# Kernel optimization log

Measured on AMD Instinct MI355X. Metric: run time of the kernel, lower is better.

The kernel has to match this reference:

```python
import jax, jax.numpy as jnp
import numpy as np

TEMP = 1.0  # temperature

def setup_inputs() -> dict:
    key = jax.random.key(0)
    ks = jax.random.split(key, 16)
    B, Cin, Cout, H, W, K, kk, A = 32, 64, 64, 128, 128, 4, 3, 16
    c_ = Cin + Cout
    r = lambda k, s: jax.random.normal(k, s, dtype=jnp.float32)
    return {
        'x': r(ks[0], (B, Cin, H, W)),
        'fc_w': r(ks[1], (A, Cin)) * 0.1,
        'ch_w': r(ks[2], (Cin, A)) * 0.1,
        'ch_b': jnp.zeros((Cin,), jnp.float32),
        'f_w': r(ks[3], (Cout, A)) * 0.1,
        'f_b': jnp.zeros((Cout,), jnp.float32),
        'sp_w': r(ks[4], (kk * kk, A)) * 0.1,
        'sp_b': jnp.zeros((kk * kk,), jnp.float32),
        'k_w': r(ks[5], (K, A)) * 0.1,
        'k_b': jnp.zeros((K,), jnp.float32),
        'fus_w1': r(ks[6], (c_ // 16, c_)) * 0.1,
        'fus_b1': jnp.zeros((c_ // 16,), jnp.float32),
        'fus_w2': r(ks[7], (c_, c_ // 16)) * 0.1,
        'fus_b2': jnp.zeros((c_,), jnp.float32),
        'weight': r(ks[8], (K, Cout, Cin, kk, kk)) * (1.0 / np.sqrt(Cin * kk * kk)),
    }

def reference(x, fc_w, ch_w, ch_b, f_w, f_b, sp_w, sp_b, k_w, k_b,
              fus_w1, fus_b1, fus_w2, fus_b2, weight):
    B, Cin, H, W = x.shape
    K, Cout, _, kk, _ = weight.shape
    # --- Attention branches (on globally pooled features) ---
    pooled = x.mean(axis=(2, 3))                      # (B, Cin)
    a = jax.nn.relu(pooled @ fc_w.T)                  # (B, A)
    ch_att = jax.nn.sigmoid(a @ ch_w.T + ch_b)        # (B, Cin)
    f_att = jax.nn.sigmoid(a @ f_w.T + f_b)           # (B, Cout)
    sp_att = jax.nn.sigmoid(a @ sp_w.T + sp_b).reshape(B, 1, 1, 1, kk, kk)
    k_att = jax.nn.softmax((a @ k_w.T + k_b) / TEMP, axis=1).reshape(B, K, 1, 1, 1, 1)
    # --- Attention fusion ---
    att = jnp.concatenate([ch_att, f_att], axis=1)    # (B, Cin+Cout)
    att2 = jax.nn.sigmoid(jax.nn.relu(att @ fus_w1.T + fus_b1) @ fus_w2.T + fus_b2)
    s1 = att2[:, :Cin].sum(axis=1)
    s2 = att2[:, Cin:].sum(axis=1)
    score = jax.nn.softmax(jnp.stack([s1, s2], axis=1) / TEMP, axis=1)
    w1 = score[:, 0][:, None, None, None]
    w2 = score[:, 1][:, None, None, None]
    # --- Apply channel attention, aggregate per-sample weights ---
    xm = w1 * x * ch_att[:, :, None, None]
    # (B,K,1,1,kk,kk)*(B,K,1,1,1,1)*(1,K,Cout,Cin,kk,kk) summed over K
    agg_w = (sp_att * k_att * weight[None]).sum(axis=1)  # (B, Cout, Cin, kk, kk)
    # --- Per-sample conv2d (stride 1, padding 1) ---
    def conv_one(xb, wb):
        return jax.lax.conv_general_dilated(
            xb[None], wb, window_strides=(1, 1), padding=[(1, 1), (1, 1)],
            dimension_numbers=('NCHW', 'OIHW', 'NCHW'))[0]
    out = jax.vmap(conv_one)(xm, agg_w)               # (B, Cout, H, W)
    return w2 * out * f_att[:, :, None, None]
```

## Files before the change

### kernel.cpp

```cpp
#include <hip/hip_runtime.h>
#include <math.h>
#include <stdint.h>

typedef short bf16x8 __attribute__((ext_vector_type(8)));
typedef float f32x16 __attribute__((ext_vector_type(16)));
typedef unsigned short ushort_t;

#define WS_POOLED 0
#define WS_CIN    2048
#define WS_COUT   4096
#define WS_SP9    6144
#define WS_K4     6432
#define WS_WF     8192

static __device__ __forceinline__ unsigned f2bf(float f) {
  unsigned u = __builtin_bit_cast(unsigned, f);
  return (u + 0x7FFFu + ((u >> 16) & 1u)) >> 16;
}
static __device__ __forceinline__ unsigned pk2(float a, float b) {
  return f2bf(a) | (f2bf(b) << 16);
}

__global__ __launch_bounds__(256) void pool_kernel(const float* __restrict__ x,
                                                   float* __restrict__ pooled) {
  const int bc = blockIdx.x;
  const int tid = threadIdx.x;
  const float4* p = (const float4*)(x + (size_t)bc * 16384);
  float s = 0.f;
  for (int j = tid; j < 4096; j += 256) {
    float4 v = p[j];
    s += (v.x + v.y) + (v.z + v.w);
  }
#pragma unroll
  for (int off = 32; off > 0; off >>= 1) s += __shfl_down(s, off, 64);
  __shared__ float red[4];
  if ((tid & 63) == 0) red[tid >> 6] = s;
  __syncthreads();
  if (tid == 0) pooled[bc] = (red[0] + red[1] + red[2] + red[3]) * (1.f / 16384.f);
}

__global__ __launch_bounds__(128) void att_kernel(
    const float* __restrict__ pooled,
    const float* __restrict__ fc_w, const float* __restrict__ ch_w, const float* __restrict__ ch_b,
    const float* __restrict__ f_w,  const float* __restrict__ f_b,
    const float* __restrict__ sp_w, const float* __restrict__ sp_b,
    const float* __restrict__ k_w,  const float* __restrict__ k_b,
    const float* __restrict__ fus_w1, const float* __restrict__ fus_b1,
    const float* __restrict__ fus_w2, const float* __restrict__ fus_b2,
    float* __restrict__ o_cin, float* __restrict__ o_cout,
    float* __restrict__ o_sp9, float* __restrict__ o_k4) {
  const int b = blockIdx.x;
  const int t = threadIdx.x;
  __shared__ float s_pool[64], s_a[16], s_att[128], s_sp[9], s_k[4], s_h[8],
      s_att2[128], s_red[2], s_w12[2];

  if (t < 64) s_pool[t] = pooled[b * 64 + t];
  __syncthreads();

  if (t < 16) {
    float s = 0.f;
    for (int c = 0; c < 64; ++c) s += s_pool[c] * fc_w[t * 64 + c];
    s_a[t] = fmaxf(s, 0.f);
  }
  __syncthreads();

  if (t < 64) {
    float s = ch_b[t];
    for (int j = 0; j < 16; ++j) s += s_a[j] * ch_w[t * 16 + j];
    s_att[t] = 1.f / (1.f + expf(-s));
  } else {
    const int o = t - 64;
    float s = f_b[o];
    for (int j = 0; j < 16; ++j) s += s_a[j] * f_w[o * 16 + j];
    s_att[t] = 1.f / (1.f + expf(-s));
  }
  if (t < 9) {
    float s = sp_b[t];
    for (int j = 0; j < 16; ++j) s += s_a[j] * sp_w[t * 16 + j];
    s_sp[t] = 1.f / (1.f + expf(-s));
  }
  if (t < 4) {
    float s = k_b[t];
    for (int j = 0; j < 16; ++j) s += s_a[j] * k_w[t * 16 + j];
    s_k[t] = s;
  }
  __syncthreads();

  if (t < 8) {
    float s = fus_b1[t];
    for (int c = 0; c < 128; ++c) s += s_att[c] * fus_w1[t * 128 + c];
    s_h[t] = fmaxf(s, 0.f);
  }
  if (t == 127) {
    float m = fmaxf(fmaxf(s_k[0], s_k[1]), fmaxf(s_k[2], s_k[3]));
    float e0 = expf(s_k[0] - m), e1 = expf(s_k[1] - m);
    float e2 = expf(s_k[2] - m), e3 = expf(s_k[3] - m);
    float inv = 1.f / (e0 + e1 + e2 + e3);
    s_k[0] = e0 * inv; s_k[1] = e1 * inv; s_k[2] = e2 * inv; s_k[3] = e3 * inv;
  }
  __syncthreads();

  {
    float s = fus_b2[t];
    for (int j = 0; j < 8; ++j) s += s_h[j] * fus_w2[t * 8 + j];
    s_att2[t] = 1.f / (1.f + expf(-s));
  }
  __syncthreads();

  if (t < 2) {
    float s = 0.f;
    for (int c = 0; c < 64; ++c) s += s_att2[t * 64 + c];
    s_red[t] = s;
  }
  __syncthreads();
  if (t == 0) {
    float m = fmaxf(s_red[0], s_red[1]);
    float e1 = expf(s_red[0] - m), e2 = expf(s_red[1] - m);
    float inv = 1.f / (e1 + e2);
    s_w12[0] = e1 * inv;
    s_w12[1] = e2 * inv;
  }
  __syncthreads();

  if (t < 64) {
    o_cin[b * 64 + t]  = s_w12[0] * s_att[t];
    o_cout[b * 64 + t] = s_w12[1] * s_att[64 + t];
  }
  if (t < 9) o_sp9[b * 9 + t] = s_sp[t];
  if (t < 4) o_k4[b * 4 + t] = s_k[t];
}

__global__ __launch_bounds__(256) void wf_kernel(const float* __restrict__ weight,
                                                 const float* __restrict__ cin,
                                                 const float* __restrict__ cout_,
                                                 const float* __restrict__ sp9,
                                                 const float* __restrict__ k4,
                                                 ushort_t* __restrict__ wfb) {
  const int bo = blockIdx.x;
  const int b = bo >> 6, o = bo & 63;
  const float co = cout_[b * 64 + o];
  const float k0 = k4[b * 4 + 0], k1 = k4[b * 4 + 1];
  const float k2 = k4[b * 4 + 2], k3 = k4[b * 4 + 3];
  for (int idx = threadIdx.x; idx < 576; idx += 256) {
    const int pq = idx >> 6, i = idx & 63;
    const size_t wi = ((size_t)o * 64 + i) * 9 + pq;
    float s = k0 * weight[wi] + k1 * weight[36864 + wi] +
              k2 * weight[73728 + wi] + k3 * weight[110592 + wi];
    float v = co * sp9[b * 9 + pq] * cin[b * 64 + i] * s;
    wfb[((size_t)(b * 9 + pq) * 64 + o) * 64 + i] = (ushort_t)f2bf(v);
  }
}

#define CONV_BUF_BYTES 26112
__global__ __launch_bounds__(512, 4) void conv_kernel(const float* __restrict__ x,
                                                      const ushort_t* __restrict__ wfb,
                                                      float* __restrict__ out) {
  const int b  = blockIdx.x >> 5;
  const int h0 = (blockIdx.x & 31) << 2;
  const int tid = threadIdx.x;
  const int lane = tid & 63;
  const int wid = tid >> 6;
  const int rw    = wid >> 1;
  const int nhalf = wid & 1;
  const int l31 = lane & 31;
  const int hi  = lane >> 5;

  __shared__ __align__(16) short sx[2 * 816 * 16];

  f32x16 acc00, acc01, acc10, acc11;
#pragma unroll
  for (int r = 0; r < 16; ++r) { acc00[r] = 0.f; acc01[r] = 0.f; acc10[r] = 0.f; acc11[r] = 0.f; }

  const ushort_t* wfb_b = wfb + (size_t)b * 9 * 64 * 64;

  const bool sact = tid < 408;
  int so = 0, sr = 0, sc = 0;
  if (sact) { so = tid / 204; const int rem = tid % 204; sr = rem / 34; sc = rem % 34; }
  const int gr  = h0 - 1 + sr;
  const int gcb = sc * 4 - 4;
  const bool inb = sact && ((unsigned)gr < 128u) && ((unsigned)gcb < 128u);
  const int pixb = sr * 136 + sc * 4;
  const int key = ((pixb >> 2) & 7) << 4;
  const int oct16 = so * 16;
  const float* xrow = x + ((size_t)b * 64) * 16384 + gr * 128 + gcb;

  float4 v0, v1, v2, v3, v4, v5, v6, v7;

#define LOADV(C0)                                              \
  do {                                                         \
    v0 = *(const float4*)(xrow + (size_t)((C0) + 0) * 16384);  \
    v1 = *(const float4*)(xrow + (size_t)((C0) + 1) * 16384);  \
    v2 = *(const float4*)(xrow + (size_t)((C0) + 2) * 16384);  \
    v3 = *(const float4*)(xrow + (size_t)((C0) + 3) * 16384);  \
    v4 = *(const float4*)(xrow + (size_t)((C0) + 4) * 16384);  \
    v5 = *(const float4*)(xrow + (size_t)((C0) + 5) * 16384);  \
    v6 = *(const float4*)(xrow + (size_t)((C0) + 6) * 16384);  \
    v7 = *(const float4*)(xrow + (size_t)((C0) + 7) * 16384);  \
  } while (0)

#define PKW(J, FLD, BUFB)                                                     \
  do {                                                                        \
    uint4 u;                                                                  \
    u.x = pk2(v0.FLD, v1.FLD);                                                \
    u.y = pk2(v2.FLD, v3.FLD);                                                \
    u.z = pk2(v4.FLD, v5.FLD);                                                \
    u.w = pk2(v6.FLD, v7.FLD);                                                \
    *(uint4*)((char*)sx + (BUFB) + ((((pixb + (J)) * 32) + oct16) ^ key)) = u;\
  } while (0)

#define PACK_WRITE(BUFB) \
  do { PKW(0, x, BUFB); PKW(1, y, BUFB); PKW(2, z, BUFB); PKW(3, w, BUFB); } while (0)

  if (sact && !inb) {
    const uint4 z = make_uint4(0u, 0u, 0u, 0u);
#pragma unroll
    for (int buf = 0; buf < 2; ++buf)
#pragma unroll
      for (int j = 0; j < 4; ++j)
        *(uint4*)((char*)sx + buf * CONV_BUF_BYTES +
                  ((((pixb + j) * 32) + oct16) ^ key)) = z;
  }

  if (inb) {
    LOADV(so * 8);
    PACK_WRITE(0);
  }
  __syncthreads();

#pragma unroll
  for (int ch = 0; ch < 4; ++ch) {
    const int c0 = ch * 16;
    if (ch < 3 && inb) LOADV(c0 + 16 + so * 8);
    const int bufb = (ch & 1) * CONV_BUF_BYTES;
#pragma unroll
    for (int p = 0; p < 3; ++p) {
#pragma unroll
      for (int q = 0; q < 3; ++q) {
        const int tap = p * 3 + q;
        bf16x8 af0 = *(const bf16x8*)(wfb_b + (tap * 64 + l31) * 64 + c0 + hi * 8);
        bf16x8 af1 = *(const bf16x8*)(wfb_b + (tap * 64 + 32 + l31) * 64 + c0 + hi * 8);
        {
          const int pix = (rw + p) * 136 + 3 + q + nhalf * 64 + l31;
          const int boff = bufb + ((pix * 32 + hi * 16) ^ (((pix >> 2) & 7) << 4));
          bf16x8 bf = *(const bf16x8*)((const char*)sx + boff);
          acc00 = __builtin_amdgcn_mfma_f32_32x32x16_bf16(af0, bf, acc00, 0, 0, 0);
          acc10 = __builtin_amdgcn_mfma_f32_32x32x16_bf16(af1, bf, acc10, 0, 0, 0);
        }
        {
          const int pix = (rw + p) * 136 + 3 + q + nhalf * 64 + 32 + l31;
          const int boff = bufb + ((pix * 32 + hi * 16) ^ (((pix >> 2) & 7) << 4));
          bf16x8 bf = *(const bf16x8*)((const char*)sx + boff);
          acc01 = __builtin_amdgcn_mfma_f32_32x32x16_bf16(af0, bf, acc01, 0, 0, 0);
          acc11 = __builtin_amdgcn_mfma_f32_32x32x16_bf16(af1, bf, acc11, 0, 0, 0);
        }
      }
    }
    if (ch < 3) {
      if (inb) PACK_WRITE(((ch + 1) & 1) * CONV_BUF_BYTES);
      __syncthreads();
    }
  }

  const int h = h0 + rw;
#define STORE_ACC(ACC, OFB, NT)                                                \
  do {                                                                         \
    const int col = nhalf * 64 + (NT) * 32 + l31;                              \
    _Pragma("unroll") for (int reg = 0; reg < 16; ++reg) {                     \
      const int o = (OFB) + (reg & 3) + ((reg >> 2) << 3) + (hi << 2);         \
      out[(((size_t)(b * 64 + o)) * 128 + h) * 128 + col] = (ACC)[reg];        \
    }                                                                          \
  } while (0)

  STORE_ACC(acc00, 0, 0);
  STORE_ACC(acc01, 0, 1);
  STORE_ACC(acc10, 32, 0);
  STORE_ACC(acc11, 32, 1);
#undef STORE_ACC
#undef PACK_WRITE
#undef PKW
#undef LOADV
}

extern "C" void kernel_launch(void* const* d_in, const int* in_sizes, int n_in,
                              void* d_out, int out_size, void* d_ws, size_t ws_size,
                              hipStream_t stream) {
  const float* x      = (const float*)d_in[0];
  const float* fc_w   = (const float*)d_in[1];
  const float* ch_w   = (const float*)d_in[2];
  const float* ch_b   = (const float*)d_in[3];
  const float* f_w    = (const float*)d_in[4];
  const float* f_b    = (const float*)d_in[5];
  const float* sp_w   = (const float*)d_in[6];
  const float* sp_b   = (const float*)d_in[7];
  const float* k_w    = (const float*)d_in[8];
  const float* k_b    = (const float*)d_in[9];
  const float* fus_w1 = (const float*)d_in[10];
  const float* fus_b1 = (const float*)d_in[11];
  const float* fus_w2 = (const float*)d_in[12];
  const float* fus_b2 = (const float*)d_in[13];
  const float* weight = (const float*)d_in[14];
  float* ws  = (float*)d_ws;
  float* out = (float*)d_out;
  ushort_t* wfb = (ushort_t*)(ws + WS_WF);

  pool_kernel<<<2048, 256, 0, stream>>>(x, ws + WS_POOLED);
  att_kernel<<<32, 128, 0, stream>>>(ws + WS_POOLED, fc_w, ch_w, ch_b, f_w, f_b,
                                     sp_w, sp_b, k_w, k_b, fus_w1, fus_b1,
                                     fus_w2, fus_b2, ws + WS_CIN, ws + WS_COUT,
                                     ws + WS_SP9, ws + WS_K4);
  wf_kernel<<<2048, 256, 0, stream>>>(weight, ws + WS_CIN, ws + WS_COUT,
                                      ws + WS_SP9, ws + WS_K4, wfb);
  conv_kernel<<<1024, 512, 0, stream>>>(x, wfb, out);
}
```

Measured before the change: 168.9 us.

## Pre-convert input to bf16 NHWC in pooling pass, stage conv from it

Replaces the pooling kernel with a convert kernel that reads x once, computes per-band partial channel sums, and writes a bf16 channel-last copy of x to workspace. The conv kernel then stages tiles with contiguous 16-byte loads from this layout instead of strided fp32 reads plus packing, and it remaps the block order. The attention kernel reduces the partial sums. This adds a bf16 write and re-read of x (about 64MB of extra traffic in total) in exchange for cheaper, coalesced conv staging.

```diff
diff --git a/kernel.cpp b/kernel.cpp
--- a/kernel.cpp
+++ b/kernel.cpp
@@ -6,12 +6,13 @@
 typedef float f32x16 __attribute__((ext_vector_type(16)));
 typedef unsigned short ushort_t;
 
-#define WS_POOLED 0
-#define WS_CIN    2048
-#define WS_COUT   4096
-#define WS_SP9    6144
-#define WS_K4     6432
-#define WS_WF     8192
+#define WP_PART 0
+#define WP_CIN  65536
+#define WP_COUT 67584
+#define WP_SP9  69632
+#define WP_K4   69920
+#define WB_WFB  294912
+#define WB_XB   2654208
 
 static __device__ __forceinline__ unsigned f2bf(float f) {
   unsigned u = __builtin_bit_cast(unsigned, f);
@@ -21,26 +22,84 @@
   return f2bf(a) | (f2bf(b) << 16);
 }
 
-__global__ __launch_bounds__(256) void pool_kernel(const float* __restrict__ x,
-                                                   float* __restrict__ pooled) {
-  const int bc = blockIdx.x;
-  const int tid = threadIdx.x;
-  const float4* p = (const float4*)(x + (size_t)bc * 16384);
-  float s = 0.f;
-  for (int j = tid; j < 4096; j += 256) {
-    float4 v = p[j];
-    s += (v.x + v.y) + (v.z + v.w);
-  }
-#pragma unroll
-  for (int off = 32; off > 0; off >>= 1) s += __shfl_down(s, off, 64);
-  __shared__ float red[4];
-  if ((tid & 63) == 0) red[tid >> 6] = s;
-  __syncthreads();
-  if (tid == 0) pooled[bc] = (red[0] + red[1] + red[2] + red[3]) * (1.f / 16384.f);
+__global__ __launch_bounds__(256) void convert_kernel(const float* __restrict__ x,
+                                                      ushort_t* __restrict__ xb,
+                                                      float* __restrict__ part) {
+  const int b    = blockIdx.x >> 5;
+  const int band = blockIdx.x & 31;
+  const int r0   = band << 2;
+  const int t    = threadIdx.x;
+  const int cp   = t & 31;
+  const int seg  = t >> 5;
+
+  __shared__ __align__(16) ushort_t tile[128 * 64];
+  __shared__ float red[512];
+
+  float sa = 0.f, sb = 0.f;
+  const float* xa  = x + ((size_t)(b * 64 + 2 * cp) * 16384);
+  const float* xb_ = xa + 16384;
+
+  for (int r = 0; r < 4; ++r) {
+    const int gr = r0 + r;
+    const int p0 = gr * 128 + seg * 16;
+    float4 a0 = *(const float4*)(xa + p0);
+    float4 a1 = *(const float4*)(xa + p0 + 4);
+    float4 a2 = *(const float4*)(xa + p0 + 8);
+    float4 a3 = *(const float4*)(xa + p0 + 12);
+    float4 b0 = *(const float4*)(xb_ + p0);
+    float4 b1 = *(const float4*)(xb_ + p0 + 4);
+    float4 b2 = *(const float4*)(xb_ + p0 + 8);
+    float4 b3 = *(const float4*)(xb_ + p0 + 12);
+    sa += (a0.x + a0.y + a0.z + a0.w) + (a1.x + a1.y + a1.z + a1.w) +
+          (a2.x + a2.y + a2.z + a2.w) + (a3.x + a3.y + a3.z + a3.w);
+    sb += (b0.x + b0.y + b0.z + b0.w) + (b1.x + b1.y + b1.z + b1.w) +
+          (b2.x + b2.y + b2.z + b2.w) + (b3.x + b3.y + b3.z + b3.w);
+
+    unsigned* tp = (unsigned*)tile;
+    const int base = seg * 16 * 32 + cp;
+    tp[base +  0 * 32] = pk2(a0.x, b0.x);
+    tp[base +  1 * 32] = pk2(a0.y, b0.y);
+    tp[base +  2 * 32] = pk2(a0.z, b0.z);
+    tp[base +  3 * 32] = pk2(a0.w, b0.w);
+    tp[base +  4 * 32] = pk2(a1.x, b1.x);
+    tp[base +  5 * 32] = pk2(a1.y, b1.y);
+    tp[base +  6 * 32] = pk2(a1.z, b1.z);
+    tp[base +  7 * 32] = pk2(a1.w, b1.w);
+    tp[base +  8 * 32] = pk2(a2.x, b2.x);
+    tp[base +  9 * 32] = pk2(a2.y, b2.y);
+    tp[base + 10 * 32] = pk2(a2.z, b2.z);
+    tp[base + 11 * 32] = pk2(a2.w, b2.w);
+    tp[base + 12 * 32] = pk2(a3.x, b3.x);
+    tp[base + 13 * 32] = pk2(a3.y, b3.y);
+    tp[base + 14 * 32] = pk2(a3.z, b3.z);
+    tp[base + 15 * 32] = pk2(a3.w, b3.w);
+    __syncthreads();
+
+    ushort_t* xbr = xb + ((size_t)(b * 16384 + gr * 128)) * 64;
+#pragma unroll
+    for (int i = 0; i < 4; ++i) {
+      const int s = i * 256 + t;
+      uint4 v = *(const uint4*)((const char*)tile + s * 16);
+      *(uint4*)(xbr + (size_t)s * 8) = v;
+    }
+    __syncthreads();
+  }
+
+  red[t] = sa;
+  red[256 + t] = sb;
+  __syncthreads();
+  if (t < 64) {
+    const int ci = t;
+    const int base = (ci & 1) * 256 + (ci >> 1);
+    float s = 0.f;
+#pragma unroll
+    for (int k = 0; k < 8; ++k) s += red[base + k * 32];
+    part[((size_t)b * 32 + band) * 64 + ci] = s;
+  }
 }
 
 __global__ __launch_bounds__(128) void att_kernel(
-    const float* __restrict__ pooled,
+    const float* __restrict__ pin, int n_part,
     const float* __restrict__ fc_w, const float* __restrict__ ch_w, const float* __restrict__ ch_b,
     const float* __restrict__ f_w,  const float* __restrict__ f_b,
     const float* __restrict__ sp_w, const float* __restrict__ sp_b,
@@ -54,7 +113,11 @@
   __shared__ float s_pool[64], s_a[16], s_att[128], s_sp[9], s_k[4], s_h[8],
       s_att2[128], s_red[2], s_w12[2];
 
-  if (t < 64) s_pool[t] = pooled[b * 64 + t];
+  if (t < 64) {
+    float s = 0.f;
+    for (int g = 0; g < n_part; ++g) s += pin[((size_t)b * n_part + g) * 64 + t];
+    s_pool[t] = s * (1.f / 16384.f);
+  }
   __syncthreads();
 
   if (t < 16) {
@@ -151,12 +214,14 @@
   }
 }
 
-#define CONV_BUF_BYTES 26112
-__global__ __launch_bounds__(512, 4) void conv_kernel(const float* __restrict__ x,
+#define TILE_BYTES 25344
+__global__ __launch_bounds__(512, 4) void conv_kernel(const ushort_t* __restrict__ xb,
                                                       const ushort_t* __restrict__ wfb,
                                                       float* __restrict__ out) {
-  const int b  = blockIdx.x >> 5;
-  const int h0 = (blockIdx.x & 31) << 2;
+  const int wg  = blockIdx.x;
+  const int swz = (wg & 7) * 128 + (wg >> 3);
+  const int b   = swz >> 5;
+  const int h0  = (swz & 31) << 2;
   const int tid = threadIdx.x;
   const int lane = tid & 63;
   const int wid = tid >> 6;
@@ -165,73 +230,60 @@
   const int l31 = lane & 31;
   const int hi  = lane >> 5;
 
-  __shared__ __align__(16) short sx[2 * 816 * 16];
+  __shared__ __align__(16) short sx[2 * 792 * 16];
 
   f32x16 acc00, acc01, acc10, acc11;
 #pragma unroll
   for (int r = 0; r < 16; ++r) { acc00[r] = 0.f; acc01[r] = 0.f; acc10[r] = 0.f; acc11[r] = 0.f; }
 
-  const ushort_t* wfb_b = wfb + (size_t)b * 9 * 64 * 64;
-
-  const bool sact = tid < 408;
-  int so = 0, sr = 0, sc = 0;
-  if (sact) { so = tid / 204; const int rem = tid % 204; sr = rem / 34; sc = rem % 34; }
-  const int gr  = h0 - 1 + sr;
-  const int gcb = sc * 4 - 4;
-  const bool inb = sact && ((unsigned)gr < 128u) && ((unsigned)gcb < 128u);
-  const int pixb = sr * 136 + sc * 4;
-  const int key = ((pixb >> 2) & 7) << 4;
-  const int oct16 = so * 16;
-  const float* xrow = x + ((size_t)b * 64) * 16384 + gr * 128 + gcb;
-
-  float4 v0, v1, v2, v3, v4, v5, v6, v7;
-
-#define LOADV(C0)                                              \
-  do {                                                         \
-    v0 = *(const float4*)(xrow + (size_t)((C0) + 0) * 16384);  \
-    v1 = *(const float4*)(xrow + (size_t)((C0) + 1) * 16384);  \
-    v2 = *(const float4*)(xrow + (size_t)((C0) + 2) * 16384);  \
-    v3 = *(const float4*)(xrow + (size_t)((C0) + 3) * 16384);  \
-    v4 = *(const float4*)(xrow + (size_t)((C0) + 4) * 16384);  \
-    v5 = *(const float4*)(xrow + (size_t)((C0) + 5) * 16384);  \
-    v6 = *(const float4*)(xrow + (size_t)((C0) + 6) * 16384);  \
-    v7 = *(const float4*)(xrow + (size_t)((C0) + 7) * 16384);  \
+  const ushort_t* wfb_b = wfb + (size_t)b * 36864;
+  const ushort_t* xb_b  = xb + (size_t)b * 16384 * 64;
+
+  int goff[4], loff[4];
+  bool act[4], inb_[4];
+#pragma unroll
+  for (int i = 0; i < 4; ++i) {
+    const int s = tid + i * 512;
+    act[i] = s < 1560;
+    const int s_ = act[i] ? s : 0;
+    const int pl = s_ >> 1, oct = s_ & 1;
+    const int r = pl / 130, tc = pl - r * 130;
+    const int gr = h0 - 1 + r, gc = tc - 1;
+    inb_[i] = act[i] && ((unsigned)gr < 128u) && ((unsigned)gc < 128u);
+    goff[i] = (gr * 128 + gc) * 64 + oct * 8;
+    const int px = r * 132 + tc;
+    const int lg = px * 32 + oct * 16;
+    loff[i] = lg ^ (((lg >> 7) & 7) << 4);
+  }
+
+  const uint4 zz = make_uint4(0u, 0u, 0u, 0u);
+  uint4 st0, st1, st2, st3;
+
+#define STAGE_LOAD(CH)                                                         \
+  do {                                                                         \
+    st0 = inb_[0] ? *(const uint4*)(xb_b + goff[0] + (CH) * 16) : zz;          \
+    st1 = inb_[1] ? *(const uint4*)(xb_b + goff[1] + (CH) * 16) : zz;          \
+    st2 = inb_[2] ? *(const uint4*)(xb_b + goff[2] + (CH) * 16) : zz;          \
+    st3 = inb_[3] ? *(const uint4*)(xb_b + goff[3] + (CH) * 16) : zz;          \
   } while (0)
 
-#define PKW(J, FLD, BUFB)                                                     \
-  do {                                                                        \
-    uint4 u;                                                                  \
-    u.x = pk2(v0.FLD, v1.FLD);                                                \
-    u.y = pk2(v2.FLD, v3.FLD);                                                \
-    u.z = pk2(v4.FLD, v5.FLD);                                                \
-    u.w = pk2(v6.FLD, v7.FLD);                                                \
-    *(uint4*)((char*)sx + (BUFB) + ((((pixb + (J)) * 32) + oct16) ^ key)) = u;\
+#define STAGE_WRITE(BUF)                                                       \
+  do {                                                                         \
+    *(uint4*)((char*)sx + (BUF) + loff[0]) = st0;                              \
+    *(uint4*)((char*)sx + (BUF) + loff[1]) = st1;                              \
+    *(uint4*)((char*)sx + (BUF) + loff[2]) = st2;                              \
+    if (act[3]) *(uint4*)((char*)sx + (BUF) + loff[3]) = st3;                  \
   } while (0)
 
-#define PACK_WRITE(BUFB) \
-  do { PKW(0, x, BUFB); PKW(1, y, BUFB); PKW(2, z, BUFB); PKW(3, w, BUFB); } while (0)
-
-  if (sact && !inb) {
-    const uint4 z = make_uint4(0u, 0u, 0u, 0u);
-#pragma unroll
-    for (int buf = 0; buf < 2; ++buf)
-#pragma unroll
-      for (int j = 0; j < 4; ++j)
-        *(uint4*)((char*)sx + buf * CONV_BUF_BYTES +
-                  ((((pixb + j) * 32) + oct16) ^ key)) = z;
-  }
-
-  if (inb) {
-    LOADV(so * 8);
-    PACK_WRITE(0);
-  }
+  STAGE_LOAD(0);
+  STAGE_WRITE(0);
   __syncthreads();
 
 #pragma unroll
   for (int ch = 0; ch < 4; ++ch) {
+    if (ch < 3) STAGE_LOAD(ch + 1);
+    const int bufb = (ch & 1) * TILE_BYTES;
     const int c0 = ch * 16;
-    if (ch < 3 && inb) LOADV(c0 + 16 + so * 8);
-    const int bufb = (ch & 1) * CONV_BUF_BYTES;
 #pragma unroll
     for (int p = 0; p < 3; ++p) {
 #pragma unroll
@@ -239,24 +291,23 @@
         const int tap = p * 3 + q;
         bf16x8 af0 = *(const bf16x8*)(wfb_b + (tap * 64 + l31) * 64 + c0 + hi * 8);
         bf16x8 af1 = *(const bf16x8*)(wfb_b + (tap * 64 + 32 + l31) * 64 + c0 + hi * 8);
+        const int pxa = (rw + p) * 132 + q + nhalf * 64 + l31;
         {
-          const int pix = (rw + p) * 136 + 3 + q + nhalf * 64 + l31;
-          const int boff = bufb + ((pix * 32 + hi * 16) ^ (((pix >> 2) & 7) << 4));
-          bf16x8 bf = *(const bf16x8*)((const char*)sx + boff);
+          const int lg = pxa * 32 + hi * 16;
+          bf16x8 bf = *(const bf16x8*)((const char*)sx + bufb + (lg ^ (((lg >> 7) & 7) << 4)));
           acc00 = __builtin_amdgcn_mfma_f32_32x32x16_bf16(af0, bf, acc00, 0, 0, 0);
           acc10 = __builtin_amdgcn_mfma_f32_32x32x16_bf16(af1, bf, acc10, 0, 0, 0);
         }
         {
-          const int pix = (rw + p) * 136 + 3 + q + nhalf * 64 + 32 + l31;
-          const int boff = bufb + ((pix * 32 + hi * 16) ^ (((pix >> 2) & 7) << 4));
-          bf16x8 bf = *(const bf16x8*)((const char*)sx + boff);
+          const int lg = (pxa + 32) * 32 + hi * 16;
+          bf16x8 bf = *(const bf16x8*)((const char*)sx + bufb + (lg ^ (((lg >> 7) & 7) << 4)));
           acc01 = __builtin_amdgcn_mfma_f32_32x32x16_bf16(af0, bf, acc01, 0, 0, 0);
           acc11 = __builtin_amdgcn_mfma_f32_32x32x16_bf16(af1, bf, acc11, 0, 0, 0);
         }
       }
     }
     if (ch < 3) {
-      if (inb) PACK_WRITE(((ch + 1) & 1) * CONV_BUF_BYTES);
+      STAGE_WRITE(((ch + 1) & 1) * TILE_BYTES);
       __syncthreads();
     }
   }
@@ -276,9 +327,8 @@
   STORE_ACC(acc10, 32, 0);
   STORE_ACC(acc11, 32, 1);
 #undef STORE_ACC
-#undef PACK_WRITE
-#undef PKW
-#undef LOADV
+#undef STAGE_WRITE
+#undef STAGE_LOAD
 }
 
 extern "C" void kernel_launch(void* const* d_in, const int* in_sizes, int n_in,
@@ -301,14 +351,19 @@
   const float* weight = (const float*)d_in[14];
   float* ws  = (float*)d_ws;
   float* out = (float*)d_out;
-  ushort_t* wfb = (ushort_t*)(ws + WS_WF);
-
-  pool_kernel<<<2048, 256, 0, stream>>>(x, ws + WS_POOLED);
-  att_kernel<<<32, 128, 0, stream>>>(ws + WS_POOLED, fc_w, ch_w, ch_b, f_w, f_b,
+
+  float* part  = ws + WP_PART;
+  float* cin   = ws + WP_CIN;
+  float* cout_ = ws + WP_COUT;
+  float* sp9   = ws + WP_SP9;
+  float* k4    = ws + WP_K4;
+  ushort_t* wfb = (ushort_t*)((char*)d_ws + WB_WFB);
+  ushort_t* xb  = (ushort_t*)((char*)d_ws + WB_XB);
+
+  convert_kernel<<<1024, 256, 0, stream>>>(x, xb, part);
+  att_kernel<<<32, 128, 0, stream>>>(part, 32, fc_w, ch_w, ch_b, f_w, f_b,
                                      sp_w, sp_b, k_w, k_b, fus_w1, fus_b1,
-                                     fus_w2, fus_b2, ws + WS_CIN, ws + WS_COUT,
-                                     ws + WS_SP9, ws + WS_K4);
-  wf_kernel<<<2048, 256, 0, stream>>>(weight, ws + WS_CIN, ws + WS_COUT,
-                                      ws + WS_SP9, ws + WS_K4, wfb);
-  conv_kernel<<<1024, 512, 0, stream>>>(x, wfb, out);
-}
+                                     fus_w2, fus_b2, cin, cout_, sp9, k4);
+  wf_kernel<<<2048, 256, 0, stream>>>(weight, cin, cout_, sp9, k4, wfb);
+  conv_kernel<<<1024, 512, 0, stream>>>(xb, wfb, out);
+}
```

Measured after the change: 171.2 us. About the same (+1.4%).
